# Kernel optimization log

Hardware: AMD Instinct MI355X
Metric: run time of the kernel (lower is better)

## Reference

```python
import jax, jax.numpy as jnp
import numpy as np

EMB, VOCAB, HID, STY = 512, 32000, 1024, 512
B, L = 32, 64

def setup_inputs() -> dict:
    key = jax.random.key(0)
    ks = jax.random.split(key, 16)
    s = 0.02  # small init to keep gates unsaturated
    return {
        'rnn_inputs': jax.random.randint(ks[0], (B, L), 0, VOCAB),
        'sentence_vector': jax.random.normal(ks[1], (B, HID), dtype=jnp.float32) * 0.1,
        'embed': jax.random.normal(ks[2], (VOCAB, EMB), dtype=jnp.float32) * s,
        'U_w': jax.random.normal(ks[3], (EMB, 4 * STY), dtype=jnp.float32) * s,
        'U_b': jnp.zeros((4 * STY,), dtype=jnp.float32),
        'S1_w': jax.random.normal(ks[4], (4 * STY, STY), dtype=jnp.float32) * s,
        'S1_b': jnp.zeros((STY,), dtype=jnp.float32),
        'V_w': jax.random.normal(ks[5], (STY, 4 * HID), dtype=jnp.float32) * s,
        'V_b': jnp.zeros((4 * HID,), dtype=jnp.float32),
        'W_w': jax.random.normal(ks[6], (HID, 4 * HID), dtype=jnp.float32) * s,
        'W_b': jnp.zeros((4 * HID,), dtype=jnp.float32),
        'P_w': jax.random.normal(ks[7], (HID, VOCAB), dtype=jnp.float32) * s,
        'P_b': jnp.zeros((VOCAB,), dtype=jnp.float32),
    }

def reference(rnn_inputs, sentence_vector, embed, U_w, U_b, S1_w, S1_b,
              V_w, V_b, W_w, W_b, P_w, P_b):
    emb = embed[rnn_inputs]                     # [B, L, E]
    xs = jnp.swapaxes(emb[:, :-1, :], 0, 1)     # time-major [L-1, B, E]
    h0 = sentence_vector
    c0 = sentence_vector

    def step(carry, x):
        h, c = carry
        U = x @ U_w + U_b                       # [B, 4*STY]
        S = U @ S1_w + S1_b                     # [B, STY]  (mode='default')
        g = (S @ V_w + V_b) + (h @ W_w + W_b)   # [B, 4*HID]
        i, f, o, cg = jnp.split(g, 4, axis=1)   # split order i, f, o, c
        c_new = jax.nn.sigmoid(f) * c + jax.nn.sigmoid(i) * jnp.tanh(cg)
        h_new = jax.nn.sigmoid(o) * c_new
        out = h_new @ P_w + P_b                 # [B, VOCAB]
        return (h_new, c_new), out

    _, outs = jax.lax.scan(step, (h0, c0), xs)  # [L-1, B, VOCAB]
    return jnp.swapaxes(outs, 0, 1)             # [B, L-1, VOCAB]
```

## Files before the change

kernel.cpp:

```cpp
#include <hip/hip_runtime.h>
#include <hip/hip_bf16.h>


typedef __bf16 bf16;
typedef bf16 bf16x8 __attribute__((ext_vector_type(8)));
typedef float f32x4 __attribute__((ext_vector_type(4)));
typedef float f32x2 __attribute__((ext_vector_type(2)));

#define NB 32
#define NL 64
#define NT 63
#define NE 512
#define NS4 2048
#define NS 512
#define NH 1024
#define NG 4096
#define NV 32000
#define MPAD 2048

#define RNB 32
#define FSTR 32

__device__ __forceinline__ float sigmoidf_(float x) { return 1.0f / (1.0f + expf(-x)); }

__device__ __forceinline__ void gload_lds16(const bf16* g, bf16* l) {
  __builtin_amdgcn_global_load_lds(
      (const __attribute__((address_space(1))) unsigned int*)g,
      (__attribute__((address_space(3))) unsigned int*)l, 16, 0, 0);
}

__device__ __forceinline__ void store_dword_wt(void* p, unsigned v) {
  asm volatile("global_store_dword %0, %1, off sc0 sc1" ::"v"(p), "v"(v) : "memory");
}

__global__ void k_transpose_cvt(const float* __restrict__ src, bf16* __restrict__ dst,
                                int R, int C) {
  __shared__ float t[32][33];
  int bx = blockIdx.x * 32;
  int by = blockIdx.y * 32;
  int tx = threadIdx.x & 31, ty = threadIdx.x >> 5;
#pragma unroll
  for (int i = 0; i < 32; i += 8)
    t[ty + i][tx] = src[(size_t)(by + ty + i) * C + (bx + tx)];
  __syncthreads();
#pragma unroll
  for (int i = 0; i < 32; i += 8)
    dst[(size_t)(bx + ty + i) * R + (by + tx)] = (bf16)t[tx][ty + i];
}

__global__ void k_gather(const int* __restrict__ rnn, const float* __restrict__ embed,
                         bf16* __restrict__ X) {
  int r = blockIdx.x;
  if (r < NB * NT) {
    int t = r >> 5, b = r & 31;
    int tok = rnn[b * NL + t];
    const float* src = embed + (size_t)tok * NE;
    for (int e = threadIdx.x; e < NE; e += 256) X[(size_t)r * NE + e] = (bf16)src[e];
  } else {
    for (int e = threadIdx.x; e < NE; e += 256) X[(size_t)r * NE + e] = (bf16)0.0f;
  }
}

__global__ void k_init(const float* __restrict__ sv, bf16* __restrict__ h0,
                       unsigned* __restrict__ flags) {
  int i = blockIdx.x * 256 + threadIdx.x;
  if (i < RNB * FSTR) flags[i] = 0u;
  if (i < NB * NH) h0[i] = (bf16)sv[i];
}

__global__ void k_bias2(const float* __restrict__ a, const float* __restrict__ b,
                        float* __restrict__ o) {
  int i = blockIdx.x * 256 + threadIdx.x;
  if (i < NG) o[i] = a[i] + b[i];
}

template <int OUT_MODE>
__global__ __launch_bounds__(256, 2) void k_gemm(const bf16* __restrict__ A,
                                                 const bf16* __restrict__ Bt,
                                                 const float* __restrict__ bias,
                                                 void* __restrict__ Cp, int K, int N) {
  __shared__ bf16 As[128 * 32];
  __shared__ bf16 Bs[128 * 32];
  const int tid = threadIdx.x;
  const int m0 = blockIdx.y * 128, n0 = blockIdx.x * 128;
  const int lane = tid & 63, w = tid >> 6;
  const int l15 = lane & 15, kq = lane >> 4;
  const int m_off = (w & 1) * 64, n_off = (w >> 1) * 64;
  const int c0 = 2 * w, c1 = 2 * w + 1;
  const int sub = lane >> 2, kkl = (lane & 3) * 8;
  const bf16* pA0 = A + (size_t)(m0 + c0 * 16 + sub) * K + kkl;
  const bf16* pA1 = A + (size_t)(m0 + c1 * 16 + sub) * K + kkl;
  const bf16* pB0 = Bt + (size_t)(n0 + c0 * 16 + sub) * K + kkl;
  const bf16* pB1 = Bt + (size_t)(n0 + c1 * 16 + sub) * K + kkl;
  f32x4 acc[4][4] = {};
  for (int k0 = 0; k0 < K; k0 += 32) {
    __syncthreads();
    gload_lds16(pA0 + k0, &As[c0 * 512]);
    gload_lds16(pA1 + k0, &As[c1 * 512]);
    gload_lds16(pB0 + k0, &Bs[c0 * 512]);
    gload_lds16(pB1 + k0, &Bs[c1 * 512]);
    __syncthreads();
    bf16x8 a[4], b[4];
#pragma unroll
    for (int i = 0; i < 4; i++)
      a[i] = *(const bf16x8*)&As[(m_off + 16 * i + l15) * 32 + kq * 8];
#pragma unroll
    for (int j = 0; j < 4; j++)
      b[j] = *(const bf16x8*)&Bs[(n_off + 16 * j + l15) * 32 + kq * 8];
#pragma unroll
    for (int i = 0; i < 4; i++)
#pragma unroll
      for (int j = 0; j < 4; j++)
        acc[i][j] = __builtin_amdgcn_mfma_f32_16x16x32_bf16(a[i], b[j], acc[i][j], 0, 0, 0);
  }
#pragma unroll
  for (int j = 0; j < 4; j++) {
    const int col = n0 + n_off + 16 * j + l15;
    const float bv = bias[col];
#pragma unroll
    for (int i = 0; i < 4; i++) {
#pragma unroll
      for (int r = 0; r < 4; r++) {
        const int row = m0 + m_off + 16 * i + kq * 4 + r;
        const float v = acc[i][j][r] + bv;
        if (OUT_MODE == 0) {
          ((bf16*)Cp)[(size_t)row * N + col] = (bf16)v;
        } else if (OUT_MODE == 1) {
          ((float*)Cp)[(size_t)row * N + col] = v;
        } else {
          if (row < NB * NT) {
            int t = row >> 5, b = row & 31;
            ((float*)Cp)[((size_t)b * NT + t) * NV + col] = v;
          }
        }
      }
    }
  }
}

__global__ __launch_bounds__(512) void k_rnn(const bf16* __restrict__ Wt,
                                             const float* __restrict__ Gx,
                                             const float* __restrict__ sv,
                                             bf16* __restrict__ hb,
                                             unsigned* __restrict__ flags) {
  __shared__ bf16 hs[32 * 1032];
  __shared__ float gl[4][32][33];
  __shared__ float cs[32][33];
  const int tid = threadIdx.x;
  const int lane = tid & 63, wid = tid >> 6;
  const int g = wid & 3, ch = wid >> 2;
  const int l15 = lane & 15, kq = lane >> 4;
  const int j0 = blockIdx.x * 32;
  const int bb_e = tid >> 4;
  const int jp = tid & 15;
  const int c0e = 2 * jp, c1e = 2 * jp + 1;

  cs[bb_e][c0e] = sv[bb_e * NH + j0 + c0e];
  cs[bb_e][c1e] = sv[bb_e * NH + j0 + c1e];

  const bf16* wrow = Wt + (size_t)(g * NH + j0 + ch * 16 + l15) * NH;
  bf16x8 breg[32];
#pragma unroll
  for (int k = 0; k < 32; k++) breg[k] = *(const bf16x8*)&wrow[k * 32 + kq * 8];

  for (int t = 0; t < NT; t++) {
    const float* gx0 = Gx + (size_t)t * NB * NG + (size_t)bb_e * NG + j0 + c0e;
    f32x2 gxr[4];
#pragma unroll
    for (int gg = 0; gg < 4; gg++) gxr[gg] = *(const f32x2*)&gx0[gg * NH];
    const bf16* hp = hb + (size_t)t * NB * NH;
#pragma unroll
    for (int q = 0; q < 8; q++) {
      int idx = tid + 512 * q;
      int row = idx >> 7, col = (idx & 127) * 8;
      *(bf16x8*)&hs[row * 1032 + col] = *(const bf16x8*)&hp[row * NH + col];
    }
    __syncthreads();
    f32x4 acc0 = {}, acc1 = {};
#pragma unroll
    for (int k = 0; k < 32; k++) {
      bf16x8 a0 = *(const bf16x8*)&hs[l15 * 1032 + k * 32 + kq * 8];
      bf16x8 a1 = *(const bf16x8*)&hs[(16 + l15) * 1032 + k * 32 + kq * 8];
      acc0 = __builtin_amdgcn_mfma_f32_16x16x32_bf16(a0, breg[k], acc0, 0, 0, 0);
      acc1 = __builtin_amdgcn_mfma_f32_16x16x32_bf16(a1, breg[k], acc1, 0, 0, 0);
    }
#pragma unroll
    for (int r = 0; r < 4; r++) {
      gl[g][kq * 4 + r][ch * 16 + l15] = acc0[r];
      gl[g][16 + kq * 4 + r][ch * 16 + l15] = acc1[r];
    }
    __syncthreads();
    {
      float hn2[2];
#pragma unroll
      for (int u = 0; u < 2; u++) {
        const int jj = c0e + u;
        float gi = gl[0][bb_e][jj] + gxr[0][u];
        float gf = gl[1][bb_e][jj] + gxr[1][u];
        float go = gl[2][bb_e][jj] + gxr[2][u];
        float gc = gl[3][bb_e][jj] + gxr[3][u];
        float cp = cs[bb_e][jj];
        float cn = sigmoidf_(gf) * cp + sigmoidf_(gi) * tanhf(gc);
        hn2[u] = sigmoidf_(go) * cn;
        cs[bb_e][jj] = cn;
      }
      unsigned short b0 = __builtin_bit_cast(unsigned short, (bf16)hn2[0]);
      unsigned short b1 = __builtin_bit_cast(unsigned short, (bf16)hn2[1]);
      unsigned pv = (unsigned)b0 | ((unsigned)b1 << 16);
      bf16* hw = hb + (size_t)(t + 1) * NB * NH + (size_t)bb_e * NH + j0 + c0e;
      store_dword_wt(hw, pv);
    }
    if (t + 1 < NT) {
      asm volatile("s_waitcnt vmcnt(0)" ::: "memory");
      __builtin_amdgcn_s_barrier();
      if (wid == 0) {
        if (lane == 0)
          __hip_atomic_store(&flags[blockIdx.x * FSTR], (unsigned)(t + 1),
                             __ATOMIC_RELAXED, __HIP_MEMORY_SCOPE_AGENT);
        const unsigned tgt = (unsigned)(t + 1);
        for (;;) {
          unsigned v = __hip_atomic_load(&flags[(lane & 31) * FSTR],
                                         __ATOMIC_RELAXED, __HIP_MEMORY_SCOPE_AGENT);
          if (__all((int)(v >= tgt))) break;
        }
      }
      __builtin_amdgcn_s_barrier();
      asm volatile("" ::: "memory");
    }
  }
}

extern "C" void kernel_launch(void* const* d_in, const int* in_sizes, int n_in,
                              void* d_out, int out_size, void* d_ws, size_t ws_size,
                              hipStream_t stream) {
  const int* rnn = (const int*)d_in[0];
  const float* sv = (const float*)d_in[1];
  const float* embed = (const float*)d_in[2];
  const float* U_w = (const float*)d_in[3];
  const float* U_b = (const float*)d_in[4];
  const float* S1_w = (const float*)d_in[5];
  const float* S1_b = (const float*)d_in[6];
  const float* V_w = (const float*)d_in[7];
  const float* V_b = (const float*)d_in[8];
  const float* W_w = (const float*)d_in[9];
  const float* W_b = (const float*)d_in[10];
  const float* P_w = (const float*)d_in[11];
  const float* P_b = (const float*)d_in[12];
  float* out = (float*)d_out;

  char* ws = (char*)d_ws;
  size_t off = 0;
  auto alloc = [&](size_t bytes) -> void* {
    void* p = ws + off;
    off += (bytes + 255) & ~(size_t)255;
    return p;
  };
  bf16* Pt = (bf16*)alloc((size_t)NV * NH * 2);
  float* Gx = (float*)alloc((size_t)MPAD * NG * 4);
  bf16* Ub = (bf16*)alloc((size_t)MPAD * NS4 * 2);
  bf16* Wt = (bf16*)alloc((size_t)NG * NH * 2);
  bf16* hb = (bf16*)alloc((size_t)(MPAD + 32) * NH * 2);
  bf16* Vt = (bf16*)alloc((size_t)NG * NS * 2);
  bf16* Xb = (bf16*)alloc((size_t)MPAD * NE * 2);
  bf16* Ut = (bf16*)alloc((size_t)NS4 * NE * 2);
  bf16* S1t = (bf16*)alloc((size_t)NS * NS4 * 2);
  bf16* Sb = (bf16*)alloc((size_t)MPAD * NS * 2);
  float* vbwb = (float*)alloc((size_t)NG * 4);
  unsigned* flags = (unsigned*)alloc((size_t)RNB * FSTR * 4);
  (void)in_sizes; (void)n_in; (void)out_size; (void)ws_size;

  k_transpose_cvt<<<dim3(NS4 / 32, NE / 32), 256, 0, stream>>>(U_w, Ut, NE, NS4);
  k_transpose_cvt<<<dim3(NS / 32, NS4 / 32), 256, 0, stream>>>(S1_w, S1t, NS4, NS);
  k_transpose_cvt<<<dim3(NG / 32, NS / 32), 256, 0, stream>>>(V_w, Vt, NS, NG);
  k_transpose_cvt<<<dim3(NG / 32, NH / 32), 256, 0, stream>>>(W_w, Wt, NH, NG);
  k_transpose_cvt<<<dim3(NV / 32, NH / 32), 256, 0, stream>>>(P_w, Pt, NH, NV);
  k_bias2<<<NG / 256, 256, 0, stream>>>(V_b, W_b, vbwb);
  k_init<<<(NB * NH + 255) / 256, 256, 0, stream>>>(sv, hb, flags);
  k_gather<<<MPAD, 256, 0, stream>>>(rnn, embed, Xb);

  k_gemm<0><<<dim3(NS4 / 128, MPAD / 128), 256, 0, stream>>>(Xb, Ut, U_b, Ub, NE, NS4);
  k_gemm<0><<<dim3(NS / 128, MPAD / 128), 256, 0, stream>>>(Ub, S1t, S1_b, Sb, NS4, NS);
  k_gemm<1><<<dim3(NG / 128, MPAD / 128), 256, 0, stream>>>(Sb, Vt, vbwb, Gx, NS, NG);

  k_rnn<<<RNB, 512, 0, stream>>>(Wt, Gx, sv, hb, flags);

  k_gemm<2><<<dim3(NV / 128, MPAD / 128), 256, 0, stream>>>(hb + (size_t)NB * NH, Pt,
                                                            P_b, out, NH, NV);
}
```

Before: 1.007 ms.

## Poll step flags in every wave and read hidden state directly from global

The recurrent kernel no longer stages the previous hidden state into shared memory behind a block barrier. Instead each wave spins on the per-block step flags, with a short sleep between polls, and then loads its MFMA operands straight from global memory. The cross-block wait moves from the end of each step to its start, so each block only publishes its flag after finishing a step. Sigmoid and tanh now use the hardware exp2 and reciprocal intrinsics. The intent is to cut the per-step barrier, the shared-memory copy latency and the transcendental cost on the serial critical path, in exchange for more polling traffic and uncached-latency global reads.

Result: slower. 1.676 ms (+66.5%).

```diff
diff --git a/kernel.cpp b/kernel.cpp
--- a/kernel.cpp
+++ b/kernel.cpp
@@ -21,7 +21,14 @@
 #define RNB 32
 #define FSTR 32
 
-__device__ __forceinline__ float sigmoidf_(float x) { return 1.0f / (1.0f + expf(-x)); }
+#define LOG2E 1.44269504088896f
+
+__device__ __forceinline__ float sigmoidf_(float x) {
+  return __builtin_amdgcn_rcpf(1.0f + __builtin_amdgcn_exp2f(-LOG2E * x));
+}
+__device__ __forceinline__ float tanhf_(float x) {
+  return 1.0f - 2.0f * __builtin_amdgcn_rcpf(1.0f + __builtin_amdgcn_exp2f(2.0f * LOG2E * x));
+}
 
 __device__ __forceinline__ void gload_lds16(const bf16* g, bf16* l) {
   __builtin_amdgcn_global_load_lds(
@@ -143,7 +150,6 @@
                                              const float* __restrict__ sv,
                                              bf16* __restrict__ hb,
                                              unsigned* __restrict__ flags) {
-  __shared__ bf16 hs[32 * 1032];
   __shared__ float gl[4][32][33];
   __shared__ float cs[32][33];
   const int tid = threadIdx.x;
@@ -153,10 +159,10 @@
   const int j0 = blockIdx.x * 32;
   const int bb_e = tid >> 4;
   const int jp = tid & 15;
-  const int c0e = 2 * jp, c1e = 2 * jp + 1;
+  const int c0e = 2 * jp;
 
   cs[bb_e][c0e] = sv[bb_e * NH + j0 + c0e];
-  cs[bb_e][c1e] = sv[bb_e * NH + j0 + c1e];
+  cs[bb_e][c0e + 1] = sv[bb_e * NH + j0 + c0e + 1];
 
   const bf16* wrow = Wt + (size_t)(g * NH + j0 + ch * 16 + l15) * NH;
   bf16x8 breg[32];
@@ -168,19 +174,25 @@
     f32x2 gxr[4];
 #pragma unroll
     for (int gg = 0; gg < 4; gg++) gxr[gg] = *(const f32x2*)&gx0[gg * NH];
-    const bf16* hp = hb + (size_t)t * NB * NH;
-#pragma unroll
-    for (int q = 0; q < 8; q++) {
-      int idx = tid + 512 * q;
-      int row = idx >> 7, col = (idx & 127) * 8;
-      *(bf16x8*)&hs[row * 1032 + col] = *(const bf16x8*)&hp[row * NH + col];
-    }
-    __syncthreads();
+
+    {
+      const unsigned tgt = (unsigned)t;
+      for (;;) {
+        unsigned v = __hip_atomic_load(&flags[(lane & 31) * FSTR],
+                                       __ATOMIC_RELAXED, __HIP_MEMORY_SCOPE_AGENT);
+        if (__all((int)(v >= tgt))) break;
+        __builtin_amdgcn_s_sleep(1);
+      }
+    }
+    asm volatile("" ::: "memory");
+
+    const bf16* hrow0 = hb + (size_t)t * NB * NH + (size_t)l15 * NH + kq * 8;
+    const bf16* hrow1 = hrow0 + 16 * NH;
     f32x4 acc0 = {}, acc1 = {};
 #pragma unroll
     for (int k = 0; k < 32; k++) {
-      bf16x8 a0 = *(const bf16x8*)&hs[l15 * 1032 + k * 32 + kq * 8];
-      bf16x8 a1 = *(const bf16x8*)&hs[(16 + l15) * 1032 + k * 32 + kq * 8];
+      bf16x8 a0 = *(const bf16x8*)(hrow0 + k * 32);
+      bf16x8 a1 = *(const bf16x8*)(hrow1 + k * 32);
       acc0 = __builtin_amdgcn_mfma_f32_16x16x32_bf16(a0, breg[k], acc0, 0, 0, 0);
       acc1 = __builtin_amdgcn_mfma_f32_16x16x32_bf16(a1, breg[k], acc1, 0, 0, 0);
     }
@@ -200,7 +212,7 @@
         float go = gl[2][bb_e][jj] + gxr[2][u];
         float gc = gl[3][bb_e][jj] + gxr[3][u];
         float cp = cs[bb_e][jj];
-        float cn = sigmoidf_(gf) * cp + sigmoidf_(gi) * tanhf(gc);
+        float cn = sigmoidf_(gf) * cp + sigmoidf_(gi) * tanhf_(gc);
         hn2[u] = sigmoidf_(go) * cn;
         cs[bb_e][jj] = cn;
       }
@@ -213,19 +225,10 @@
     if (t + 1 < NT) {
       asm volatile("s_waitcnt vmcnt(0)" ::: "memory");
       __builtin_amdgcn_s_barrier();
-      if (wid == 0) {
-        if (lane == 0)
-          __hip_atomic_store(&flags[blockIdx.x * FSTR], (unsigned)(t + 1),
-                             __ATOMIC_RELAXED, __HIP_MEMORY_SCOPE_AGENT);
-        const unsigned tgt = (unsigned)(t + 1);
-        for (;;) {
-          unsigned v = __hip_atomic_load(&flags[(lane & 31) * FSTR],
-                                         __ATOMIC_RELAXED, __HIP_MEMORY_SCOPE_AGENT);
-          if (__all((int)(v >= tgt))) break;
-        }
-      }
+      if (wid == 0 && lane == 0)
+        __hip_atomic_store(&flags[blockIdx.x * FSTR], (unsigned)(t + 1),
+                           __ATOMIC_RELAXED, __HIP_MEMORY_SCOPE_AGENT);
       __builtin_amdgcn_s_barrier();
-      asm volatile("" ::: "memory");
     }
   }
 }
```
